# Optimization experiments

Hardware: AMD Instinct MI355X
Metric: run time of the kernel (lower is better)

Reference implementation:

```python
import jax, jax.numpy as jnp
import numpy as np

MAX_STEPS = 20  # matches init kwarg max_steps


def gru_cell(x, h, W_ih, W_hh, b_ih, b_hh):
    # PyTorch GRUCell: gates ordered (reset, update, new)
    H = h.shape[1]
    gx = x @ W_ih.T + b_ih          # [B, 3H]
    gh = h @ W_hh.T + b_hh          # [B, 3H]
    r = jax.nn.sigmoid(gx[:, :H] + gh[:, :H])
    z = jax.nn.sigmoid(gx[:, H:2 * H] + gh[:, H:2 * H])
    n = jnp.tanh(gx[:, 2 * H:] + r * gh[:, 2 * H:])
    return (1.0 - z) * n + z * h


def setup_inputs() -> dict:
    key = jax.random.key(0)
    ks = jax.random.split(key, 10)
    B, E, H = 2048, 512, 1024
    bound = 1.0 / np.sqrt(H)  # torch default init scale
    uni = lambda k, shape: jax.random.uniform(k, shape, jnp.float32, -bound, bound)
    return {
        "x": jax.random.normal(ks[0], (B, E), jnp.float32),
        "W_ih": uni(ks[1], (3 * H, E)),
        "W_hh": uni(ks[2], (3 * H, H)),
        "b_ih": uni(ks[3], (3 * H,)),
        "b_hh": uni(ks[4], (3 * H,)),
        "w_out": uni(ks[5], (H,)),
        "b_out": uni(ks[6], (1,)),
        "w_lam": uni(ks[7], (H,)),
        "b_lam": uni(ks[8], (1,)),
        "u": jax.random.uniform(ks[9], (MAX_STEPS, B), jnp.float32),  # bernoulli draws
    }


def reference(x, W_ih, W_hh, b_ih, b_hh, w_out, b_out, w_lam, b_lam, u):
    B = x.shape[0]
    dt = x.dtype
    H = W_hh.shape[1]
    h0 = gru_cell(x, jnp.zeros((B, H), dt), W_ih, W_hh, b_ih, b_hh)
    steps = jnp.arange(1, MAX_STEPS + 1)

    def step(carry, inp):
        h, un_halted, halted, p_m, y_m = carry
        n_idx, u_n = inp
        lam_sig = jax.nn.sigmoid(h @ w_lam + b_lam[0])           # [B]
        lam = jnp.where(n_idx == MAX_STEPS, jnp.ones_like(lam_sig), lam_sig)
        y_n = h @ w_out + b_out[0]                                # [B]
        p_n = un_halted * lam
        un_halted = un_halted * (1.0 - lam)
        halt = (u_n < lam).astype(dt) * (1.0 - halted)            # bernoulli(lam)
        p_m = p_m * (1.0 - halt) + p_n * halt
        y_m = y_m * (1.0 - halt) + y_n * halt
        halted = halted + halt
        h = gru_cell(x, h, W_ih, W_hh, b_ih, b_hh)
        return (h, un_halted, halted, p_m, y_m), (p_n, y_n)

    init = (h0,
            jnp.ones((B,), dt),
            jnp.zeros((B,), dt),
            jnp.zeros((B,), dt),
            jnp.zeros((B,), dt))
    (_, _, _, p_m, y_m), (p, y) = jax.lax.scan(step, init, (steps, u))
    return p, y, p_m, y_m
```

## Files before the change

### kernel.cpp

```cpp
#include <hip/hip_runtime.h>
#include <math.h>


#define B_N 2048
#define E_N 512
#define H_N 1024
#define G3  3072
#define NSTEPS 20
#define BK 32
#define NT_H (H_N / BK)
#define NT_E (E_N / BK)
#define NCB  (H_N / 64)

typedef __attribute__((ext_vector_type(8))) _Float16 f16x8;
typedef __attribute__((ext_vector_type(4))) _Float16 f16x4v;
typedef __attribute__((ext_vector_type(4))) float    f32x4;

#define GLDS(src, dst) \
  __builtin_amdgcn_global_load_lds( \
      (const __attribute__((address_space(1))) void*)(src), \
      (__attribute__((address_space(3))) void*)(dst), 16, 0, 0)

__device__ __forceinline__ float sigmoidf_(float x) { return 1.0f / (1.0f + expf(-x)); }

__global__ __launch_bounds__(256, 1)
void gemm_step_mfma(const _Float16* __restrict__ h_hi_in,
                    const _Float16* __restrict__ h_lo_in,
                    const _Float16* __restrict__ Whi,
                    const _Float16* __restrict__ Wlo,
                    const float* __restrict__ b_hh,
                    const float* __restrict__ gx,
                    const float* __restrict__ w_lam,
                    const float* __restrict__ w_out,
                    _Float16* __restrict__ h_hi_out,
                    _Float16* __restrict__ h_lo_out,
                    float* __restrict__ part_lam,
                    float* __restrict__ part_out)
{
  __shared__ _Float16 lds[2][20480];
  __shared__ float pl_red[128][2], po_red[128][2];

  const int tid  = threadIdx.x;
  const int lane = tid & 63;
  const int wv   = tid >> 6;
  const int wr   = wv >> 1;
  const int wc   = wv & 1;
  const int row0 = blockIdx.y * 128;
  const int col0 = blockIdx.x * 64;
  const int cb   = blockIdx.x;

  const int lrow = lane & 15;
  const int q    = lane >> 4;

  const _Float16* srcp[10];
  int ldsoff[10];
  {
    const int row16 = lane >> 2;
    const int seg_e = ((lane & 3) ^ (row16 & 3) ^ ((row16 >> 2) & 3)) * 8;
    #pragma unroll
    for (int j = 0; j < 10; ++j) {
      const int c = wv * 10 + j;
      const _Float16* s;
      if (c < 8) {
        s = h_hi_in + (size_t)(row0 + c * 16 + row16) * H_N + seg_e;
      } else if (c < 16) {
        const int cc = c - 8;
        s = h_lo_in + (size_t)(row0 + cc * 16 + row16) * H_N + seg_e;
      } else if (c < 28) {
        const int cc = c - 16;
        const int wrow = (cc >> 2) * H_N + col0 + (cc & 3) * 16 + row16;
        s = Whi + (size_t)wrow * H_N + seg_e;
      } else {
        const int cc = c - 28;
        const int wrow = (cc >> 2) * H_N + col0 + (cc & 3) * 16 + row16;
        s = Wlo + (size_t)wrow * H_N + seg_e;
      }
      srcp[j]   = s;
      ldsoff[j] = c * 512;
    }
  }

  const int rdoff = (4 * lrow + (q ^ (lrow & 3) ^ ((lrow >> 2) & 3))) * 8;

  f32x4 acc[3][4][2];
  #pragma unroll
  for (int g = 0; g < 3; ++g)
    #pragma unroll
    for (int mi = 0; mi < 4; ++mi)
      #pragma unroll
      for (int ni = 0; ni < 2; ++ni)
        acc[g][mi][ni] = (f32x4){0.f, 0.f, 0.f, 0.f};

  auto issue = [&](int p) {
    #pragma unroll
    for (int j = 0; j < 10; ++j) { GLDS(srcp[j], &lds[p][ldsoff[j]]); srcp[j] += BK; }
  };

  issue(0);
  __syncthreads();

  for (int t = 0; t < NT_H; ++t) {
    const int p = t & 1;
    if (t + 1 < NT_H) issue(p ^ 1);

    const _Float16* Lp = &lds[p][0];

    f16x8 ah[4], al[4];
    #pragma unroll
    for (int mi = 0; mi < 4; ++mi) {
      ah[mi] = *(const f16x8*)&Lp[(wr * 4 + mi) * 512 + rdoff];
      al[mi] = *(const f16x8*)&Lp[(8 + wr * 4 + mi) * 512 + rdoff];
    }
    f16x8 bh[3][2], bl[3][2];
    #pragma unroll
    for (int g = 0; g < 3; ++g)
      #pragma unroll
      for (int ni = 0; ni < 2; ++ni) {
        bh[g][ni] = *(const f16x8*)&Lp[(16 + g * 4 + wc * 2 + ni) * 512 + rdoff];
        bl[g][ni] = *(const f16x8*)&Lp[(28 + g * 4 + wc * 2 + ni) * 512 + rdoff];
      }

    #pragma unroll
    for (int g = 0; g < 3; ++g)
      #pragma unroll
      for (int mi = 0; mi < 4; ++mi)
        #pragma unroll
        for (int ni = 0; ni < 2; ++ni) {
          f32x4 c = acc[g][mi][ni];
          c = __builtin_amdgcn_mfma_f32_16x16x32_f16(ah[mi], bh[g][ni], c, 0, 0, 0);
          c = __builtin_amdgcn_mfma_f32_16x16x32_f16(ah[mi], bl[g][ni], c, 0, 0, 0);
          c = __builtin_amdgcn_mfma_f32_16x16x32_f16(al[mi], bh[g][ni], c, 0, 0, 0);
          acc[g][mi][ni] = c;
        }
    __syncthreads();
  }

  #pragma unroll
  for (int mi = 0; mi < 4; ++mi) {
    float plr[4] = {0.f, 0.f, 0.f, 0.f};
    float por[4] = {0.f, 0.f, 0.f, 0.f};
    #pragma unroll
    for (int ni = 0; ni < 2; ++ni) {
      const int n = col0 + wc * 32 + ni * 16 + lrow;
      const float bhr = b_hh[n];
      const float bhz = b_hh[H_N + n];
      const float bhn = b_hh[2 * H_N + n];
      const float wl  = w_lam[n];
      const float wo  = w_out[n];
      #pragma unroll
      for (int r = 0; r < 4; ++r) {
        const int m = row0 + wr * 64 + mi * 16 + q * 4 + r;
        const float gr = acc[0][mi][ni][r] + bhr;
        const float gz = acc[1][mi][ni][r] + bhz;
        const float gn = acc[2][mi][ni][r] + bhn;
        const size_t gxb = (size_t)m * G3;
        const float rr = sigmoidf_(gx[gxb + n] + gr);
        const float zz = sigmoidf_(gx[gxb + H_N + n] + gz);
        const float nn = tanhf(gx[gxb + 2 * H_N + n] + rr * gn);
        const size_t hidx = (size_t)m * H_N + n;
        const float hold = (float)h_hi_in[hidx] + (float)h_lo_in[hidx];
        const float hf = (1.f - zz) * nn + zz * hold;
        const _Float16 hh = (_Float16)hf;
        h_hi_out[hidx] = hh;
        h_lo_out[hidx] = (_Float16)(hf - (float)hh);
        plr[r] += hf * wl;
        por[r] += hf * wo;
      }
    }
    #pragma unroll
    for (int r = 0; r < 4; ++r) {
      float pl = plr[r], po = por[r];
      #pragma unroll
      for (int mk = 1; mk < 16; mk <<= 1) {
        pl += __shfl_xor(pl, mk);
        po += __shfl_xor(po, mk);
      }
      if (lrow == 0) {
        pl_red[wr * 64 + mi * 16 + q * 4 + r][wc] = pl;
        po_red[wr * 64 + mi * 16 + q * 4 + r][wc] = po;
      }
    }
  }
  __syncthreads();
  if (tid < 128) {
    const int m = row0 + tid;
    part_lam[(size_t)cb * B_N + m] = pl_red[tid][0] + pl_red[tid][1];
    part_out[(size_t)cb * B_N + m] = po_red[tid][0] + po_red[tid][1];
  }
}

__global__ __launch_bounds__(256, 3)
void gemm_gx_mfma(const _Float16* __restrict__ xhi,
                  const _Float16* __restrict__ xlo,
                  const _Float16* __restrict__ Wihhi,
                  const _Float16* __restrict__ Wihlo,
                  const float* __restrict__ b_ih,
                  float* __restrict__ gx)
{
  __shared__ _Float16 lds[2][12288];

  const int tid  = threadIdx.x;
  const int lane = tid & 63;
  const int wv   = tid >> 6;
  const int wr   = wv >> 1;
  const int wc   = wv & 1;
  const int row0 = blockIdx.y * 128;
  const int col0 = blockIdx.x * 64;

  const _Float16* srcp[6];
  int ldsoff[6];
  #pragma unroll
  for (int j = 0; j < 6; ++j) {
    const int c     = wv * 6 + j;
    const int seg   = (lane & 3) * 8;
    const int row16 = lane >> 2;
    const _Float16* s;
    if (c < 8)       s = xhi   + (size_t)(row0 + c * 16 + row16) * E_N + seg;
    else if (c < 16) s = xlo   + (size_t)(row0 + (c - 8) * 16 + row16) * E_N + seg;
    else if (c < 20) s = Wihhi + (size_t)(col0 + (c - 16) * 16 + row16) * E_N + seg;
    else             s = Wihlo + (size_t)(col0 + (c - 20) * 16 + row16) * E_N + seg;
    srcp[j]   = s;
    ldsoff[j] = c * 512;
  }

  f32x4 acc[4][2];
  #pragma unroll
  for (int mi = 0; mi < 4; ++mi)
    #pragma unroll
    for (int ni = 0; ni < 2; ++ni) acc[mi][ni] = (f32x4){0.f, 0.f, 0.f, 0.f};

  const int lrow = lane & 15;
  const int lk   = (lane >> 4) * 8;
  const int q    = lane >> 4;

  #pragma unroll
  for (int j = 0; j < 6; ++j) { GLDS(srcp[j], &lds[0][ldsoff[j]]); srcp[j] += BK; }
  __syncthreads();

  for (int t = 0; t < NT_E; ++t) {
    const int p = t & 1;
    if (t + 1 < NT_E) {
      #pragma unroll
      for (int j = 0; j < 6; ++j) { GLDS(srcp[j], &lds[p ^ 1][ldsoff[j]]); srcp[j] += BK; }
    }
    f16x8 ah[4], al[4];
    #pragma unroll
    for (int mi = 0; mi < 4; ++mi) {
      const int r = wr * 64 + mi * 16 + lrow;
      ah[mi] = *(const f16x8*)&lds[p][r * 32 + lk];
      al[mi] = *(const f16x8*)&lds[p][4096 + r * 32 + lk];
    }
    f16x8 bh[2], bl[2];
    #pragma unroll
    for (int ni = 0; ni < 2; ++ni) {
      const int r = wc * 32 + ni * 16 + lrow;
      bh[ni] = *(const f16x8*)&lds[p][8192 + r * 32 + lk];
      bl[ni] = *(const f16x8*)&lds[p][10240 + r * 32 + lk];
    }
    #pragma unroll
    for (int mi = 0; mi < 4; ++mi)
      #pragma unroll
      for (int ni = 0; ni < 2; ++ni) {
        f32x4 c = acc[mi][ni];
        c = __builtin_amdgcn_mfma_f32_16x16x32_f16(ah[mi], bh[ni], c, 0, 0, 0);
        c = __builtin_amdgcn_mfma_f32_16x16x32_f16(ah[mi], bl[ni], c, 0, 0, 0);
        c = __builtin_amdgcn_mfma_f32_16x16x32_f16(al[mi], bh[ni], c, 0, 0, 0);
        acc[mi][ni] = c;
      }
    __syncthreads();
  }

  #pragma unroll
  for (int mi = 0; mi < 4; ++mi) {
    #pragma unroll
    for (int ni = 0; ni < 2; ++ni) {
      const int n = col0 + wc * 32 + ni * 16 + lrow;
      const float bi = b_ih[n];
      #pragma unroll
      for (int r = 0; r < 4; ++r) {
        const int m = row0 + wr * 64 + mi * 16 + q * 4 + r;
        gx[(size_t)m * G3 + n] = acc[mi][ni][r] + bi;
      }
    }
  }
}

__global__ __launch_bounds__(256)
void split_f32_kernel(const float* __restrict__ src,
                      _Float16* __restrict__ hi, _Float16* __restrict__ lo)
{
  const size_t base = ((size_t)blockIdx.x * 256 + threadIdx.x) * 4;
  const float4 w = *(const float4*)&src[base];
  float s[4] = {w.x, w.y, w.z, w.w};
  f16x4v h4, l4;
  #pragma unroll
  for (int e = 0; e < 4; ++e) {
    const _Float16 h = (_Float16)s[e];
    h4[e] = h;
    l4[e] = (_Float16)(s[e] - (float)h);
  }
  *(f16x4v*)&hi[base] = h4;
  *(f16x4v*)&lo[base] = l4;
}

__global__ __launch_bounds__(256)
void init_h0_kernel(const float* __restrict__ gx, const float* __restrict__ b_hh,
                    _Float16* __restrict__ h_hi, _Float16* __restrict__ h_lo,
                    float* __restrict__ states)
{
    const int idx = blockIdx.x * 256 + threadIdx.x;
    const int r = idx >> 10;
    const int c = idx & (H_N - 1);
    const float rr = sigmoidf_(gx[(size_t)r * G3 + c] + b_hh[c]);
    const float zz = sigmoidf_(gx[(size_t)r * G3 + H_N + c] + b_hh[H_N + c]);
    const float nn = tanhf(gx[(size_t)r * G3 + 2 * H_N + c] + rr * b_hh[2 * H_N + c]);
    const float hf = (1.0f - zz) * nn;
    const _Float16 hh = (_Float16)hf;
    h_hi[idx] = hh;
    h_lo[idx] = (_Float16)(hf - (float)hh);
    if (idx < B_N) {
        states[idx]           = 1.0f;
        states[B_N + idx]     = 0.0f;
        states[2 * B_N + idx] = 0.0f;
        states[3 * B_N + idx] = 0.0f;
    }
}

__global__ __launch_bounds__(256)
void halt_kernel(const int n,
                 const _Float16* __restrict__ h_hi, const _Float16* __restrict__ h_lo,
                 const float* __restrict__ w_out, const float* __restrict__ b_out,
                 const float* __restrict__ w_lam, const float* __restrict__ b_lam,
                 const float* __restrict__ u,
                 float* __restrict__ states,
                 float* __restrict__ out_p, float* __restrict__ out_y,
                 float* __restrict__ out_pm, float* __restrict__ out_ym)
{
    const int row = blockIdx.x;
    const int tid = threadIdx.x;
    const size_t base = (size_t)row * H_N + (tid << 2);
    const f16x4v hh4 = *(const f16x4v*)&h_hi[base];
    const f16x4v hl4 = *(const f16x4v*)&h_lo[base];
    const float4 wl = *(const float4*)&w_lam[tid << 2];
    const float4 wo = *(const float4*)&w_out[tid << 2];
    float hv[4];
    #pragma unroll
    for (int e = 0; e < 4; ++e) hv[e] = (float)hh4[e] + (float)hl4[e];
    float s_lam = hv[0] * wl.x + hv[1] * wl.y + hv[2] * wl.z + hv[3] * wl.w;
    float s_out = hv[0] * wo.x + hv[1] * wo.y + hv[2] * wo.z + hv[3] * wo.w;
    #pragma unroll
    for (int off = 32; off > 0; off >>= 1) {
        s_lam += __shfl_down(s_lam, off);
        s_out += __shfl_down(s_out, off);
    }
    __shared__ float redl[4], redo[4];
    const int wid = tid >> 6;
    if ((tid & 63) == 0) { redl[wid] = s_lam; redo[wid] = s_out; }
    __syncthreads();
    if (tid == 0) {
        const float dlam = redl[0] + redl[1] + redl[2] + redl[3];
        const float dout = redo[0] + redo[1] + redo[2] + redo[3];
        const float lam = (n == NSTEPS) ? 1.0f : sigmoidf_(dlam + b_lam[0]);
        const float y_n = dout + b_out[0];
        float un = states[row];
        float ha = states[B_N + row];
        float pm = states[2 * B_N + row];
        float ym = states[3 * B_N + row];
        const float p_n = un * lam;
        un = un * (1.0f - lam);
        const float halt = (u[(size_t)(n - 1) * B_N + row] < lam ? 1.0f : 0.0f) * (1.0f - ha);
        pm = pm * (1.0f - halt) + p_n * halt;
        ym = ym * (1.0f - halt) + y_n * halt;
        ha += halt;
        states[row] = un;
        states[B_N + row] = ha;
        states[2 * B_N + row] = pm;
        states[3 * B_N + row] = ym;
        out_p[(size_t)(n - 1) * B_N + row] = p_n;
        out_y[(size_t)(n - 1) * B_N + row] = y_n;
        if (n == NSTEPS) { out_pm[row] = pm; out_ym[row] = ym; }
    }
}

__global__ __launch_bounds__(256)
void finish_halt_kernel(const int n,
                        const float* __restrict__ part_lam,
                        const float* __restrict__ part_out,
                        const float* __restrict__ b_out, const float* __restrict__ b_lam,
                        const float* __restrict__ u,
                        float* __restrict__ states,
                        float* __restrict__ out_p, float* __restrict__ out_y,
                        float* __restrict__ out_pm, float* __restrict__ out_ym)
{
    const int row = blockIdx.x * 256 + threadIdx.x;
    float dlam = 0.f, dout = 0.f;
    #pragma unroll
    for (int cb = 0; cb < NCB; ++cb) {
        dlam += part_lam[(size_t)cb * B_N + row];
        dout += part_out[(size_t)cb * B_N + row];
    }
    const float lam = (n == NSTEPS) ? 1.0f : sigmoidf_(dlam + b_lam[0]);
    const float y_n = dout + b_out[0];
    float un = states[row];
    float ha = states[B_N + row];
    float pm = states[2 * B_N + row];
    float ym = states[3 * B_N + row];
    const float p_n = un * lam;
    un = un * (1.0f - lam);
    const float halt = (u[(size_t)(n - 1) * B_N + row] < lam ? 1.0f : 0.0f) * (1.0f - ha);
    pm = pm * (1.0f - halt) + p_n * halt;
    ym = ym * (1.0f - halt) + y_n * halt;
    ha += halt;
    states[row] = un;
    states[B_N + row] = ha;
    states[2 * B_N + row] = pm;
    states[3 * B_N + row] = ym;
    out_p[(size_t)(n - 1) * B_N + row] = p_n;
    out_y[(size_t)(n - 1) * B_N + row] = y_n;
    if (n == NSTEPS) { out_pm[row] = pm; out_ym[row] = ym; }
}

extern "C" void kernel_launch(void* const* d_in, const int* in_sizes, int n_in,
                              void* d_out, int out_size, void* d_ws, size_t ws_size,
                              hipStream_t stream) {
    const float* x     = (const float*)d_in[0];
    const float* W_ih  = (const float*)d_in[1];
    const float* W_hh  = (const float*)d_in[2];
    const float* b_ih  = (const float*)d_in[3];
    const float* b_hh  = (const float*)d_in[4];
    const float* w_out = (const float*)d_in[5];
    const float* b_out = (const float*)d_in[6];
    const float* w_lam = (const float*)d_in[7];
    const float* b_lam = (const float*)d_in[8];
    const float* u     = (const float*)d_in[9];

    float* out_p  = (float*)d_out;
    float* out_y  = out_p + (size_t)NSTEPS * B_N;
    float* out_pm = out_y + (size_t)NSTEPS * B_N;
    float* out_ym = out_pm + B_N;

    float* ws = (float*)d_ws;
    float*     gx   = ws;
    _Float16*  Whi  = (_Float16*)(gx + (size_t)B_N * G3);
    _Float16*  Wlo  = Whi + (size_t)G3 * H_N;
    _Float16*  hAhi = Wlo + (size_t)G3 * H_N;
    _Float16*  hAlo = hAhi + (size_t)B_N * H_N;
    _Float16*  hBhi = hAlo + (size_t)B_N * H_N;
    _Float16*  hBlo = hBhi + (size_t)B_N * H_N;
    float*     part_lam = (float*)(hBlo + (size_t)B_N * H_N);
    float*     part_out = part_lam + (size_t)NCB * B_N;
    float*     states   = part_out + (size_t)NCB * B_N;

    const dim3 blk(256);
    split_f32_kernel<<<dim3((size_t)G3 * H_N / 1024), blk, 0, stream>>>(W_hh, Whi, Wlo);
    split_f32_kernel<<<dim3((size_t)G3 * E_N / 1024), blk, 0, stream>>>(W_ih, hAhi, hAlo);
    split_f32_kernel<<<dim3((size_t)B_N * E_N / 1024), blk, 0, stream>>>(x, hBhi, hBlo);
    gemm_gx_mfma<<<dim3(G3 / 64, B_N / 128), blk, 0, stream>>>(hBhi, hBlo, hAhi, hAlo, b_ih, gx);
    init_h0_kernel<<<dim3(B_N * H_N / 256), blk, 0, stream>>>(gx, b_hh, hAhi, hAlo, states);

    _Float16 *hchi = hAhi, *hclo = hAlo, *hnhi = hBhi, *hnlo = hBlo;
    for (int n = 1; n <= NSTEPS; ++n) {
        if (n == 1) {
            halt_kernel<<<dim3(B_N), blk, 0, stream>>>(n, hchi, hclo, w_out, b_out,
                                                       w_lam, b_lam, u, states,
                                                       out_p, out_y, out_pm, out_ym);
        } else {
            finish_halt_kernel<<<dim3(B_N / 256), blk, 0, stream>>>(n, part_lam, part_out,
                                                                    b_out, b_lam, u, states,
                                                                    out_p, out_y, out_pm, out_ym);
        }
        if (n < NSTEPS) {
            gemm_step_mfma<<<dim3(H_N / 64, B_N / 128), blk, 0, stream>>>(
                hchi, hclo, Whi, Wlo, b_hh, gx, w_lam, w_out, hnhi, hnlo, part_lam, part_out);
            _Float16* t;
            t = hchi; hchi = hnhi; hnhi = t;
            t = hclo; hclo = hnlo; hnlo = t;
        }
    }
}
```

Baseline: 1.488 ms.

## Fuse per-step halting update into recurrent GEMM kernel and drop LDS swizzle

The per-step finish_halt_kernel launch is folded into the next gemm_step_mfma launch. Blocks in column 0 reduce the previous step's partial lam/out sums and update the halting state while the first tile loads are in flight. The partial-sum buffers are double-buffered so the reads and writes of consecutive steps do not collide, and one separate kernel handles the final step. Separately, the XOR swizzle on LDS tile placement and reads is replaced by a plain row-major layout. That layout is simpler but risks more LDS bank conflicts in the MFMA operand loads.

```diff
diff --git a/kernel.cpp b/kernel.cpp
--- a/kernel.cpp
+++ b/kernel.cpp
@@ -24,7 +24,8 @@
 __device__ __forceinline__ float sigmoidf_(float x) { return 1.0f / (1.0f + expf(-x)); }
 
 __global__ __launch_bounds__(256, 1)
-void gemm_step_mfma(const _Float16* __restrict__ h_hi_in,
+void gemm_step_mfma(const int n, const int do_halt,
+                    const _Float16* __restrict__ h_hi_in,
                     const _Float16* __restrict__ h_lo_in,
                     const _Float16* __restrict__ Whi,
                     const _Float16* __restrict__ Wlo,
@@ -32,10 +33,16 @@
                     const float* __restrict__ gx,
                     const float* __restrict__ w_lam,
                     const float* __restrict__ w_out,
+                    const float* __restrict__ b_out, const float* __restrict__ b_lam,
+                    const float* __restrict__ u,
                     _Float16* __restrict__ h_hi_out,
                     _Float16* __restrict__ h_lo_out,
-                    float* __restrict__ part_lam,
-                    float* __restrict__ part_out)
+                    const float* __restrict__ part_lam_in,
+                    const float* __restrict__ part_out_in,
+                    float* __restrict__ part_lam_out,
+                    float* __restrict__ part_out_out,
+                    float* __restrict__ states,
+                    float* __restrict__ out_p, float* __restrict__ out_y)
 {
   __shared__ _Float16 lds[2][20480];
   __shared__ float pl_red[128][2], po_red[128][2];
@@ -49,38 +56,28 @@
   const int col0 = blockIdx.x * 64;
   const int cb   = blockIdx.x;
 
-  const int lrow = lane & 15;
-  const int q    = lane >> 4;
-
   const _Float16* srcp[10];
   int ldsoff[10];
-  {
+  #pragma unroll
+  for (int j = 0; j < 10; ++j) {
+    const int c     = wv * 10 + j;
+    const int seg   = (lane & 3) * 8;
     const int row16 = lane >> 2;
-    const int seg_e = ((lane & 3) ^ (row16 & 3) ^ ((row16 >> 2) & 3)) * 8;
-    #pragma unroll
-    for (int j = 0; j < 10; ++j) {
-      const int c = wv * 10 + j;
-      const _Float16* s;
-      if (c < 8) {
-        s = h_hi_in + (size_t)(row0 + c * 16 + row16) * H_N + seg_e;
-      } else if (c < 16) {
-        const int cc = c - 8;
-        s = h_lo_in + (size_t)(row0 + cc * 16 + row16) * H_N + seg_e;
-      } else if (c < 28) {
-        const int cc = c - 16;
-        const int wrow = (cc >> 2) * H_N + col0 + (cc & 3) * 16 + row16;
-        s = Whi + (size_t)wrow * H_N + seg_e;
-      } else {
-        const int cc = c - 28;
-        const int wrow = (cc >> 2) * H_N + col0 + (cc & 3) * 16 + row16;
-        s = Wlo + (size_t)wrow * H_N + seg_e;
-      }
-      srcp[j]   = s;
-      ldsoff[j] = c * 512;
-    }
-  }
-
-  const int rdoff = (4 * lrow + (q ^ (lrow & 3) ^ ((lrow >> 2) & 3))) * 8;
+    const _Float16* s;
+    if (c < 8) {
+      s = h_hi_in + (size_t)(row0 + c * 16 + row16) * H_N + seg;
+    } else if (c < 16) {
+      s = h_lo_in + (size_t)(row0 + (c - 8) * 16 + row16) * H_N + seg;
+    } else if (c < 28) {
+      const int br = (c - 16) * 16 + row16;
+      s = Whi + (size_t)((br >> 6) * H_N + col0 + (br & 63)) * H_N + seg;
+    } else {
+      const int br = (c - 28) * 16 + row16;
+      s = Wlo + (size_t)((br >> 6) * H_N + col0 + (br & 63)) * H_N + seg;
+    }
+    srcp[j]   = s;
+    ldsoff[j] = c * 512;
+  }
 
   f32x4 acc[3][4][2];
   #pragma unroll
@@ -91,35 +88,65 @@
       for (int ni = 0; ni < 2; ++ni)
         acc[g][mi][ni] = (f32x4){0.f, 0.f, 0.f, 0.f};
 
+  const int lrow = lane & 15;
+  const int lk   = (lane >> 4) * 8;
+  const int q    = lane >> 4;
+
   auto issue = [&](int p) {
     #pragma unroll
     for (int j = 0; j < 10; ++j) { GLDS(srcp[j], &lds[p][ldsoff[j]]); srcp[j] += BK; }
   };
 
   issue(0);
+  if (do_halt && cb == 0 && tid < 128) {
+    const int row = row0 + tid;
+    float dlam = 0.f, dout = 0.f;
+    #pragma unroll
+    for (int cq = 0; cq < NCB; ++cq) {
+      dlam += part_lam_in[(size_t)cq * B_N + row];
+      dout += part_out_in[(size_t)cq * B_N + row];
+    }
+    const float lam = sigmoidf_(dlam + b_lam[0]);
+    const float y_n = dout + b_out[0];
+    float un = states[row];
+    float ha = states[B_N + row];
+    float pm = states[2 * B_N + row];
+    float ym = states[3 * B_N + row];
+    const float p_n = un * lam;
+    un = un * (1.0f - lam);
+    const float halt = (u[(size_t)(n - 1) * B_N + row] < lam ? 1.0f : 0.0f) * (1.0f - ha);
+    pm = pm * (1.0f - halt) + p_n * halt;
+    ym = ym * (1.0f - halt) + y_n * halt;
+    ha += halt;
+    states[row] = un;
+    states[B_N + row] = ha;
+    states[2 * B_N + row] = pm;
+    states[3 * B_N + row] = ym;
+    out_p[(size_t)(n - 1) * B_N + row] = p_n;
+    out_y[(size_t)(n - 1) * B_N + row] = y_n;
+  }
   __syncthreads();
 
   for (int t = 0; t < NT_H; ++t) {
     const int p = t & 1;
     if (t + 1 < NT_H) issue(p ^ 1);
 
-    const _Float16* Lp = &lds[p][0];
-
     f16x8 ah[4], al[4];
     #pragma unroll
     for (int mi = 0; mi < 4; ++mi) {
-      ah[mi] = *(const f16x8*)&Lp[(wr * 4 + mi) * 512 + rdoff];
-      al[mi] = *(const f16x8*)&Lp[(8 + wr * 4 + mi) * 512 + rdoff];
+      const int r = wr * 64 + mi * 16 + lrow;
+      ah[mi] = *(const f16x8*)&lds[p][r * 32 + lk];
+      al[mi] = *(const f16x8*)&lds[p][4096 + r * 32 + lk];
     }
     f16x8 bh[3][2], bl[3][2];
     #pragma unroll
     for (int g = 0; g < 3; ++g)
       #pragma unroll
       for (int ni = 0; ni < 2; ++ni) {
-        bh[g][ni] = *(const f16x8*)&Lp[(16 + g * 4 + wc * 2 + ni) * 512 + rdoff];
-        bl[g][ni] = *(const f16x8*)&Lp[(28 + g * 4 + wc * 2 + ni) * 512 + rdoff];
+        const int r = g * 64 + wc * 32 + ni * 16 + lrow;
+        bh[g][ni] = *(const f16x8*)&lds[p][8192 + r * 32 + lk];
+        bl[g][ni] = *(const f16x8*)&lds[p][14336 + r * 32 + lk];
       }
-
     #pragma unroll
     for (int g = 0; g < 3; ++g)
       #pragma unroll
@@ -141,12 +168,12 @@
     float por[4] = {0.f, 0.f, 0.f, 0.f};
     #pragma unroll
     for (int ni = 0; ni < 2; ++ni) {
-      const int n = col0 + wc * 32 + ni * 16 + lrow;
-      const float bhr = b_hh[n];
-      const float bhz = b_hh[H_N + n];
-      const float bhn = b_hh[2 * H_N + n];
-      const float wl  = w_lam[n];
-      const float wo  = w_out[n];
+      const int nn_ = col0 + wc * 32 + ni * 16 + lrow;
+      const float bhr = b_hh[nn_];
+      const float bhz = b_hh[H_N + nn_];
+      const float bhn = b_hh[2 * H_N + nn_];
+      const float wl  = w_lam[nn_];
+      const float wo  = w_out[nn_];
       #pragma unroll
       for (int r = 0; r < 4; ++r) {
         const int m = row0 + wr * 64 + mi * 16 + q * 4 + r;
@@ -154,10 +181,10 @@
         const float gz = acc[1][mi][ni][r] + bhz;
         const float gn = acc[2][mi][ni][r] + bhn;
         const size_t gxb = (size_t)m * G3;
-        const float rr = sigmoidf_(gx[gxb + n] + gr);
-        const float zz = sigmoidf_(gx[gxb + H_N + n] + gz);
-        const float nn = tanhf(gx[gxb + 2 * H_N + n] + rr * gn);
-        const size_t hidx = (size_t)m * H_N + n;
+        const float rr = sigmoidf_(gx[gxb + nn_] + gr);
+        const float zz = sigmoidf_(gx[gxb + H_N + nn_] + gz);
+        const float nn = tanhf(gx[gxb + 2 * H_N + nn_] + rr * gn);
+        const size_t hidx = (size_t)m * H_N + nn_;
         const float hold = (float)h_hi_in[hidx] + (float)h_lo_in[hidx];
         const float hf = (1.f - zz) * nn + zz * hold;
         const _Float16 hh = (_Float16)hf;
@@ -184,8 +211,8 @@
   __syncthreads();
   if (tid < 128) {
     const int m = row0 + tid;
-    part_lam[(size_t)cb * B_N + m] = pl_red[tid][0] + pl_red[tid][1];
-    part_out[(size_t)cb * B_N + m] = po_red[tid][0] + po_red[tid][1];
+    part_lam_out[(size_t)cb * B_N + m] = pl_red[tid][0] + pl_red[tid][1];
+    part_out_out[(size_t)cb * B_N + m] = po_red[tid][0] + po_red[tid][1];
   }
 }
 
@@ -447,9 +474,11 @@
     _Float16*  hAlo = hAhi + (size_t)B_N * H_N;
     _Float16*  hBhi = hAlo + (size_t)B_N * H_N;
     _Float16*  hBlo = hBhi + (size_t)B_N * H_N;
-    float*     part_lam = (float*)(hBlo + (size_t)B_N * H_N);
-    float*     part_out = part_lam + (size_t)NCB * B_N;
-    float*     states   = part_out + (size_t)NCB * B_N;
+    float*     pl0  = (float*)(hBlo + (size_t)B_N * H_N);
+    float*     po0  = pl0 + (size_t)NCB * B_N;
+    float*     pl1  = po0 + (size_t)NCB * B_N;
+    float*     po1  = pl1 + (size_t)NCB * B_N;
+    float*     states = po1 + (size_t)NCB * B_N;
 
     const dim3 blk(256);
     split_f32_kernel<<<dim3((size_t)G3 * H_N / 1024), blk, 0, stream>>>(W_hh, Whi, Wlo);
@@ -458,23 +487,25 @@
     gemm_gx_mfma<<<dim3(G3 / 64, B_N / 128), blk, 0, stream>>>(hBhi, hBlo, hAhi, hAlo, b_ih, gx);
     init_h0_kernel<<<dim3(B_N * H_N / 256), blk, 0, stream>>>(gx, b_hh, hAhi, hAlo, states);
 
+    halt_kernel<<<dim3(B_N), blk, 0, stream>>>(1, hAhi, hAlo, w_out, b_out,
+                                               w_lam, b_lam, u, states,
+                                               out_p, out_y, out_pm, out_ym);
+
     _Float16 *hchi = hAhi, *hclo = hAlo, *hnhi = hBhi, *hnlo = hBlo;
-    for (int n = 1; n <= NSTEPS; ++n) {
-        if (n == 1) {
-            halt_kernel<<<dim3(B_N), blk, 0, stream>>>(n, hchi, hclo, w_out, b_out,
-                                                       w_lam, b_lam, u, states,
-                                                       out_p, out_y, out_pm, out_ym);
-        } else {
-            finish_halt_kernel<<<dim3(B_N / 256), blk, 0, stream>>>(n, part_lam, part_out,
-                                                                    b_out, b_lam, u, states,
-                                                                    out_p, out_y, out_pm, out_ym);
-        }
-        if (n < NSTEPS) {
-            gemm_step_mfma<<<dim3(H_N / 64, B_N / 128), blk, 0, stream>>>(
-                hchi, hclo, Whi, Wlo, b_hh, gx, w_lam, w_out, hnhi, hnlo, part_lam, part_out);
-            _Float16* t;
-            t = hchi; hchi = hnhi; hnhi = t;
-            t = hclo; hclo = hnlo; hnlo = t;
-        }
-    }
-}
+    for (int n = 1; n <= NSTEPS - 1; ++n) {
+        float* pli = ((n - 1) & 1) ? pl1 : pl0;
+        float* poi = ((n - 1) & 1) ? po1 : po0;
+        float* plo = (n & 1) ? pl1 : pl0;
+        float* poo = (n & 1) ? po1 : po0;
+        gemm_step_mfma<<<dim3(H_N / 64, B_N / 128), blk, 0, stream>>>(
+            n, (n >= 2) ? 1 : 0,
+            hchi, hclo, Whi, Wlo, b_hh, gx, w_lam, w_out, b_out, b_lam, u,
+            hnhi, hnlo, pli, poi, plo, poo, states, out_p, out_y);
+        _Float16* t;
+        t = hchi; hchi = hnhi; hnhi = t;
+        t = hclo; hclo = hnlo; hnlo = t;
+    }
+    finish_halt_kernel<<<dim3(B_N / 256), blk, 0, stream>>>(NSTEPS, pl1, po1,
+                                                            b_out, b_lam, u, states,
+                                                            out_p, out_y, out_pm, out_ym);
+}
```

Measured after the change: 1.360 ms. 1.09x faster.
